# Optimization experiments

Hardware: AMD Instinct MI355X
Metric: run time of the kernel (lower is better)

Reference implementation:

```python
import jax, jax.numpy as jnp
import numpy as np

B, NF, EC, H, W = 16, 64, 3, 256, 256
NF1, NF2 = NF // 8, NF // 4  # 8, 16

def _leaky(x):
    return jnp.where(x >= 0, x, 0.2 * x)

def setup_inputs() -> dict:
    key = jax.random.key(0)
    ks = jax.random.split(key, 10)
    s = lambda fan_in: 1.0 / np.sqrt(fan_in)
    return {
        "feature_maps": jax.random.normal(ks[0], (B, NF, H, W), dtype=jnp.float32),
        "extra_maps": jax.random.normal(ks[1], (B, EC, H, W), dtype=jnp.float32),
        "w1": jax.random.uniform(ks[2], (NF1, EC), jnp.float32, -s(EC), s(EC)),
        "b1": jax.random.uniform(ks[3], (NF1,), jnp.float32, -s(EC), s(EC)),
        "w2": jax.random.uniform(ks[4], (NF2, NF1), jnp.float32, -s(NF1), s(NF1)),
        "b2": jax.random.uniform(ks[5], (NF2,), jnp.float32, -s(NF1), s(NF1)),
        "wm": jax.random.uniform(ks[6], (NF, NF2), jnp.float32, -s(NF2), s(NF2)),
        "bm": jax.random.uniform(ks[7], (NF,), jnp.float32, -s(NF2), s(NF2)),
        "wa": jax.random.uniform(ks[8], (NF, NF2), jnp.float32, -s(NF2), s(NF2)),
        "ba": jax.random.uniform(ks[9], (NF,), jnp.float32, -s(NF2), s(NF2)),
    }

def reference(feature_maps, extra_maps, w1, b1, w2, b2, wm, bm, wa, ba):
    # 1x1 convs expressed as channel contractions (per-pixel MLP chain)
    fea1 = _leaky(jnp.einsum('oc,bchw->bohw', w1, extra_maps) + b1[:, None, None])
    fea2 = _leaky(jnp.einsum('oc,bchw->bohw', w2, fea1) + b2[:, None, None])
    mul = jnp.einsum('oc,bchw->bohw', wm, fea2) + bm[:, None, None]
    add = jnp.einsum('oc,bchw->bohw', wa, fea2) + ba[:, None, None]
    # out = add / (1 + feature_maps * mul)
    return add / (1.0 + feature_maps * mul)
```

## Files before the change

### kernel.cpp

```cpp
#include <hip/hip_runtime.h>

#define HW 65536
#define NPIX (16 * HW)
#define THREADS 256


#define DW1 0
#define DB1 24
#define DW2 32
#define DB2 160
#define DWM 176
#define DBM 1200
#define NDBL 1264
#define FWA 0
#define FBA 1024

__device__ __forceinline__ double leakyd(double x) {
    return fmax(x, 0.2 * x);
}

__global__ __launch_bounds__(256) void cvt_weights(
    const float* __restrict__ w1, const float* __restrict__ b1,
    const float* __restrict__ w2, const float* __restrict__ b2,
    const float* __restrict__ wm, const float* __restrict__ bm,
    const float* __restrict__ wa, const float* __restrict__ ba,
    double* __restrict__ wd, float* __restrict__ wf)
{
    const int t = threadIdx.x;
    if (t < 24)  wd[DW1 + t] = (double)w1[t];
    if (t < 8)   wd[DB1 + t] = (double)b1[t];
    if (t < 128) wd[DW2 + t] = (double)w2[t];
    if (t < 16)  wd[DB2 + t] = (double)b2[t];
    if (t < 64)  wd[DBM + t] = (double)bm[t];
    if (t < 64)  wf[FBA + t] = ba[t];
    #pragma unroll
    for (int i = 0; i < 4; ++i) {
        wd[DWM + t + i * 256] = (double)wm[t + i * 256];
        wf[FWA + t + i * 256] = wa[t + i * 256];
    }
}

__global__ __launch_bounds__(THREADS, 4) void attcnn_kernel(
    const float* __restrict__ fm,
    const float* __restrict__ ex,
    const double* __restrict__ wd,
    const float* __restrict__ wf,
    float* __restrict__ out)
{
    const int idx = blockIdx.x * THREADS + threadIdx.x;
    const int b   = idx >> 16;
    const int hw  = idx & 65535;

    const float* exp_ = ex + (long)b * 3 * HW + hw;
    const double e0 = (double)exp_[0];
    const double e1 = (double)exp_[HW];
    const double e2 = (double)exp_[2 * HW];

    double f1v[8];
    #pragma unroll
    for (int j = 0; j < 8; ++j) {
        f1v[j] = leakyd(fma(wd[DW1 + j * 3 + 0], e0,
                        fma(wd[DW1 + j * 3 + 1], e1,
                        fma(wd[DW1 + j * 3 + 2], e2, wd[DB1 + j]))));
    }

    double f2d[16];
    float  f2s[16];
    #pragma unroll
    for (int k = 0; k < 16; ++k) {
        double acc = wd[DB2 + k];
        #pragma unroll
        for (int j = 0; j < 8; ++j)
            acc = fma(wd[DW2 + k * 8 + j], f1v[j], acc);
        acc = leakyd(acc);
        f2d[k] = acc;
        f2s[k] = (float)acc;
    }

    const float* fmp = fm  + (long)b * 64 * HW + hw;
    float*       op  = out + (long)b * 64 * HW + hw;

    float fcur[8], fnxt[8];
    #pragma unroll
    for (int i = 0; i < 8; ++i)
        fcur[i] = __builtin_nontemporal_load(fmp + (long)i * HW);

    #pragma unroll 1
    for (int c = 0; c < 8; ++c) {
        const int ob = c * 8;
        if (c < 7) {
            #pragma unroll
            for (int i = 0; i < 8; ++i)
                fnxt[i] = __builtin_nontemporal_load(fmp + (long)(ob + 8 + i) * HW);
        }
        #pragma unroll
        for (int i = 0; i < 8; ++i) {
            const int o = ob + i;
            const double* wmr = wd + DWM + o * 16;
            const float*  war = wf + FWA + o * 16;
            double m0 = wd[DBM + o], m1 = 0.0;
            float  a0 = wf[FBA + o], a1 = 0.0f;
            #pragma unroll
            for (int k = 0; k < 16; k += 2) {
                m0 = fma(wmr[k],     f2d[k],     m0);
                m1 = fma(wmr[k + 1], f2d[k + 1], m1);
                a0 = fmaf(war[k],     f2s[k],     a0);
                a1 = fmaf(war[k + 1], f2s[k + 1], a1);
            }
            const double m = m0 + m1;
            const float  a = a0 + a1;
            const double den = fma((double)fcur[i], m, 1.0);
            float h = (float)den;
            float r = __builtin_amdgcn_rcpf(h);
            r = r * fmaf(-h, r, 2.0f);
            __builtin_nontemporal_store(a * r, op + (long)o * HW);
        }
        if (c < 7) {
            #pragma unroll
            for (int i = 0; i < 8; ++i) fcur[i] = fnxt[i];
        }
    }
}

extern "C" void kernel_launch(void* const* d_in, const int* in_sizes, int n_in,
                              void* d_out, int out_size, void* d_ws, size_t ws_size,
                              hipStream_t stream) {
    const float* fm = (const float*)d_in[0];
    const float* ex = (const float*)d_in[1];
    const float* w1 = (const float*)d_in[2];
    const float* b1 = (const float*)d_in[3];
    const float* w2 = (const float*)d_in[4];
    const float* b2 = (const float*)d_in[5];
    const float* wm = (const float*)d_in[6];
    const float* bm = (const float*)d_in[7];
    const float* wa = (const float*)d_in[8];
    const float* ba = (const float*)d_in[9];
    float* out = (float*)d_out;

    double* wd = (double*)d_ws;
    float*  wf = (float*)(wd + NDBL);

    cvt_weights<<<1, 256, 0, stream>>>(w1, b1, w2, b2, wm, bm, wa, ba, wd, wf);

    const int blocks = NPIX / THREADS;
    attcnn_kernel<<<blocks, THREADS, 0, stream>>>(fm, ex, wd, wf, out);
}
```

Baseline: 463.4 us.

## Fully unroll channel loop with 16-deep load prefetch and packed float2 FMAs

Replaces the 8-channel chunked loop with a fully unrolled 64-channel loop. Feature-map loads are issued 16 channels ahead, and the first 16 loads are hoisted before the MLP prologue so their latency overlaps the double-precision compute. The float 'add' branch now uses packed two-wide FMAs (v2f elementwise fma), which could map to packed FP32 instructions. The deeper prefetch and the 64-entry register array raise VGPR pressure, which may cut occupancy under the launch bound of 4 blocks or cause spills.

```diff
diff --git a/kernel.cpp b/kernel.cpp
--- a/kernel.cpp
+++ b/kernel.cpp
@@ -14,6 +14,8 @@
 #define NDBL 1264
 #define FWA 0
 #define FBA 1024
+
+typedef float v2f __attribute__((ext_vector_type(2)));
 
 __device__ __forceinline__ double leakyd(double x) {
     return fmax(x, 0.2 * x);
@@ -52,9 +54,21 @@
     const int hw  = idx & 65535;
 
     const float* exp_ = ex + (long)b * 3 * HW + hw;
-    const double e0 = (double)exp_[0];
-    const double e1 = (double)exp_[HW];
-    const double e2 = (double)exp_[2 * HW];
+    const float* fmp  = fm  + (long)b * 64 * HW + hw;
+    float*       op   = out + (long)b * 64 * HW + hw;
+
+    const float ex0 = exp_[0];
+    const float ex1 = exp_[HW];
+    const float ex2 = exp_[2 * HW];
+
+    float fv[64];
+    #pragma unroll
+    for (int i = 0; i < 16; ++i)
+        fv[i] = __builtin_nontemporal_load(fmp + (long)i * HW);
+
+    const double e0 = (double)ex0;
+    const double e1 = (double)ex1;
+    const double e2 = (double)ex2;
 
     double f1v[8];
     #pragma unroll
@@ -65,60 +79,48 @@
     }
 
     double f2d[16];
-    float  f2s[16];
     #pragma unroll
     for (int k = 0; k < 16; ++k) {
         double acc = wd[DB2 + k];
         #pragma unroll
         for (int j = 0; j < 8; ++j)
             acc = fma(wd[DW2 + k * 8 + j], f1v[j], acc);
-        acc = leakyd(acc);
-        f2d[k] = acc;
-        f2s[k] = (float)acc;
+        f2d[k] = leakyd(acc);
+    }
+    v2f f2p[8];
+    #pragma unroll
+    for (int k2 = 0; k2 < 8; ++k2) {
+        f2p[k2].x = (float)f2d[2 * k2];
+        f2p[k2].y = (float)f2d[2 * k2 + 1];
     }
 
-    const float* fmp = fm  + (long)b * 64 * HW + hw;
-    float*       op  = out + (long)b * 64 * HW + hw;
+    #pragma unroll
+    for (int o = 0; o < 64; ++o) {
+        if (o + 16 < 64)
+            fv[o + 16] = __builtin_nontemporal_load(fmp + (long)(o + 16) * HW);
 
-    float fcur[8], fnxt[8];
-    #pragma unroll
-    for (int i = 0; i < 8; ++i)
-        fcur[i] = __builtin_nontemporal_load(fmp + (long)i * HW);
+        const double* wmr = wd + DWM + o * 16;
+        const v2f*    war = (const v2f*)(wf + FWA + o * 16);
 
-    #pragma unroll 1
-    for (int c = 0; c < 8; ++c) {
-        const int ob = c * 8;
-        if (c < 7) {
-            #pragma unroll
-            for (int i = 0; i < 8; ++i)
-                fnxt[i] = __builtin_nontemporal_load(fmp + (long)(ob + 8 + i) * HW);
+        double m0 = wd[DBM + o], m1 = 0.0;
+        #pragma unroll
+        for (int k = 0; k < 16; k += 2) {
+            m0 = fma(wmr[k],     f2d[k],     m0);
+            m1 = fma(wmr[k + 1], f2d[k + 1], m1);
         }
+        const double m = m0 + m1;
+
+        v2f av = { wf[FBA + o], 0.0f };
         #pragma unroll
-        for (int i = 0; i < 8; ++i) {
-            const int o = ob + i;
-            const double* wmr = wd + DWM + o * 16;
-            const float*  war = wf + FWA + o * 16;
-            double m0 = wd[DBM + o], m1 = 0.0;
-            float  a0 = wf[FBA + o], a1 = 0.0f;
-            #pragma unroll
-            for (int k = 0; k < 16; k += 2) {
-                m0 = fma(wmr[k],     f2d[k],     m0);
-                m1 = fma(wmr[k + 1], f2d[k + 1], m1);
-                a0 = fmaf(war[k],     f2s[k],     a0);
-                a1 = fmaf(war[k + 1], f2s[k + 1], a1);
-            }
-            const double m = m0 + m1;
-            const float  a = a0 + a1;
-            const double den = fma((double)fcur[i], m, 1.0);
-            float h = (float)den;
-            float r = __builtin_amdgcn_rcpf(h);
-            r = r * fmaf(-h, r, 2.0f);
-            __builtin_nontemporal_store(a * r, op + (long)o * HW);
-        }
-        if (c < 7) {
-            #pragma unroll
-            for (int i = 0; i < 8; ++i) fcur[i] = fnxt[i];
-        }
+        for (int k2 = 0; k2 < 8; ++k2)
+            av = __builtin_elementwise_fma(war[k2], f2p[k2], av);
+        const float a = av.x + av.y;
+
+        const double den = fma((double)fv[o], m, 1.0);
+        float h = (float)den;
+        float r = __builtin_amdgcn_rcpf(h);
+        r = r * fmaf(-h, r, 2.0f);
+        __builtin_nontemporal_store(a * r, op + (long)o * HW);
     }
 }
 
```

Measured after the change: 462.2 us. About the same (-0.3%).
